# Optimization experiments

Measured on AMD Instinct MI355X. Metric: run time of the kernel, lower is better.

The kernel has to match this reference:

```python
import jax, jax.numpy as jnp
import numpy as np

LN_EPS = 1e-5

def _cell(x, h, c, Wih, Whh, bih, bhh):
    # PyTorch LSTMCell: gate order i, f, g, o
    z = x @ Wih.T + h @ Whh.T + bih + bhh
    i, f, g, o = jnp.split(z, 4, axis=-1)
    c = jax.nn.sigmoid(f) * c + jax.nn.sigmoid(i) * jnp.tanh(g)
    h = jax.nn.sigmoid(o) * jnp.tanh(c)
    return h, c

def _forward(encoder_inputs, decoder_inputs, enc_Wih, enc_Whh, enc_bih, enc_bhh,
             dec_Wih, dec_Whh, dec_bih, dec_bhh, attn_in_w, attn_in_b,
             attn_out_w, attn_out_b, ln_g, ln_b, out_w, out_b):
    B = encoder_inputs.shape[0]
    H = enc_Whh.shape[1]
    Sd = decoder_inputs.shape[1]
    h0 = jnp.zeros((B, H), encoder_inputs.dtype)
    c0 = jnp.zeros((B, H), encoder_inputs.dtype)

    def enc_step(carry, x_t):
        h, c = _cell(x_t, carry[0], carry[1], enc_Wih, enc_Whh, enc_bih, enc_bhh)
        return (h, c), h

    (h_e, c_e), hs = jax.lax.scan(enc_step, (h0, c0), jnp.swapaxes(encoder_inputs, 0, 1))
    enc_out = jnp.swapaxes(hs, 0, 1)  # [B, Se, H]

    # MultiheadAttention (1 head): precompute K, V once since keys/values are static
    Wq, Wk, Wv = jnp.split(attn_in_w, 3, axis=0)
    bq, bk, bv = jnp.split(attn_in_b, 3)
    K = enc_out @ Wk.T + bk  # [B, Se, H]
    V = enc_out @ Wv.T + bv  # [B, Se, H]
    scale = 1.0 / float(np.sqrt(H))

    def dec_step(carry, _):
        h, c, x = carry
        h, c = _cell(x, h, c, dec_Wih, dec_Whh, dec_bih, dec_bhh)
        q = h @ Wq.T + bq  # [B, H], single query per step
        attn = jax.nn.softmax(jnp.einsum('bh,bsh->bs', q, K) * scale, axis=-1)
        ctx = jnp.einsum('bs,bsh->bh', attn, V) @ attn_out_w.T + attn_out_b
        y = ctx + h  # residual with raw (pre-projection) query, as in the torch code
        mu = jnp.mean(y, axis=-1, keepdims=True)
        var = jnp.mean((y - mu) ** 2, axis=-1, keepdims=True)
        y = (y - mu) * jax.lax.rsqrt(var + LN_EPS) * ln_g + ln_b
        out = y @ out_w.T + out_b  # [B, 1]
        return (h, c, out), out

    init = (h_e, c_e, decoder_inputs[:, 0, :])
    _, outs = jax.lax.scan(dec_step, init, None, length=Sd)
    return jnp.swapaxes(outs, 0, 1)  # [B, Sd, 1]

def setup_inputs():
    key = jax.random.key(0)
    ks = jax.random.split(key, 13)
    B, Se, Sd, H, O = 64, 512, 128, 512, 1
    s = 1.0 / float(np.sqrt(H))
    def p(k, shape, sc):
        return (jax.random.uniform(k, shape, jnp.float32) * 2.0 - 1.0) * sc
    return {
        "encoder_inputs": jax.random.normal(ks[0], (B, Se, 1), jnp.float32),
        "decoder_inputs": jax.random.normal(ks[1], (B, Sd, 1), jnp.float32),
        "enc_Wih": p(ks[2], (4 * H, 1), s), "enc_Whh": p(ks[3], (4 * H, H), s),
        "enc_bih": p(ks[4], (4 * H,), s), "enc_bhh": p(ks[5], (4 * H,), s),
        "dec_Wih": p(ks[6], (4 * H, 1), s), "dec_Whh": p(ks[7], (4 * H, H), s),
        "dec_bih": p(ks[8], (4 * H,), s), "dec_bhh": p(ks[9], (4 * H,), s),
        "attn_in_w": p(ks[10], (3 * H, H), s),
        "attn_in_b": jnp.zeros((3 * H,), jnp.float32),
        "attn_out_w": p(ks[11], (H, H), s),
        "attn_out_b": jnp.zeros((H,), jnp.float32),
        "ln_g": jnp.ones((H,), jnp.float32), "ln_b": jnp.zeros((H,), jnp.float32),
        "out_w": p(ks[12], (O, H), s), "out_b": jnp.zeros((O,), jnp.float32),
    }

def reference(encoder_inputs, decoder_inputs, enc_Wih, enc_Whh, enc_bih, enc_bhh,
              dec_Wih, dec_Whh, dec_bih, dec_bhh, attn_in_w, attn_in_b,
              attn_out_w, attn_out_b, ln_g, ln_b, out_w, out_b):
    return _forward(encoder_inputs, decoder_inputs, enc_Wih, enc_Whh, enc_bih, enc_bhh,
                    dec_Wih, dec_Whh, dec_bih, dec_bhh, attn_in_w, attn_in_b,
                    attn_out_w, attn_out_b, ln_g, ln_b, out_w, out_b)
```

## Files before the change

kernel.cpp:

```cpp
#include <hip/hip_runtime.h>
#include <hip/hip_bf16.h>
#include <stdint.h>


#define HID 512
#define NBAT 64
#define SEQE 512
#define SEQD 128
#define NGRP 4
#define GBAT 16
#define GBLK 64
#define NH 8
#define SCALE 0.04419417382415922f
#define FLS 16

typedef __attribute__((ext_vector_type(8))) short bf16x8;
typedef __attribute__((ext_vector_type(4))) float f32x4;
#define MFMA_B16 __builtin_amdgcn_mfma_f32_16x16x32_bf16

static constexpr size_t OFF_G   = 0;
static constexpr size_t OFF_NM  = OFF_G  + (size_t)HID*HID*4;
static constexpr size_t OFF_M0  = OFF_NM + (size_t)HID*HID*4;
static constexpr size_t OFF_N0  = OFF_M0 + 2048;
static constexpr size_t OFF_WQB = OFF_N0 + 2048;
static constexpr size_t OFF_SC  = OFF_WQB + 2048;
static constexpr size_t OFF_HB  = OFF_SC + 256;
static constexpr size_t OFF_CB  = OFF_HB + (size_t)3*NBAT*HID*4;
static constexpr size_t OFF_EBP = OFF_CB + (size_t)NBAT*HID*4;
static constexpr size_t OFF_MD  = OFF_EBP + (size_t)NBAT*4*HID*4;
static constexpr size_t OFF_KB  = OFF_MD + (size_t)NBAT*4*4;
static constexpr size_t OFF_FLG = OFF_KB + (size_t)NBAT*SEQE*4;
static constexpr size_t OFF_XPK = OFF_FLG + (size_t)3*NGRP*GBLK*FLS*4;
static constexpr size_t OFF_BFK = ((OFF_XPK + 512 + 255) & ~(size_t)255);
static constexpr size_t OFF_BFV = OFF_BFK + (size_t)16*32*64*8*2;
static constexpr size_t OFF_EO  = OFF_BFV + (size_t)16*32*64*8*2;
static constexpr size_t OFF_VT  = OFF_EO + (size_t)NBAT*SEQE*HID*2;

__device__ __forceinline__ float bf2f(uint32_t u) {
  union { float f; uint32_t i; } x; x.i = u << 16; return x.f;
}
__device__ __forceinline__ unsigned short bfbits(float f) {
  __hip_bfloat16 h = __float2bfloat16(f);
  return *(unsigned short*)&h;
}
__device__ __forceinline__ uint32_t splitbf(float f) {
  unsigned short hi = bfbits(f);
  union { uint32_t u; float ff; } c; c.u = (uint32_t)hi << 16;
  unsigned short lo = bfbits(f - c.ff);
  return (uint32_t)hi | ((uint32_t)lo << 16);
}
__device__ __forceinline__ float sigm(float x) { return 1.f / (1.f + __expf(-x)); }

__device__ __forceinline__ void stg(float* p, float v) {
  __hip_atomic_store(p, v, __ATOMIC_RELAXED, __HIP_MEMORY_SCOPE_AGENT);
}
__device__ __forceinline__ void stgu(uint32_t* p, uint32_t v) {
  __hip_atomic_store(p, v, __ATOMIC_RELAXED, __HIP_MEMORY_SCOPE_AGENT);
}
__device__ __forceinline__ void stgi(int* p, int v) {
  __hip_atomic_store(p, v, __ATOMIC_RELAXED, __HIP_MEMORY_SCOPE_AGENT);
}
__device__ __forceinline__ void stg64(unsigned long long* p, unsigned long long v) {
  __hip_atomic_store(p, v, __ATOMIC_RELAXED, __HIP_MEMORY_SCOPE_AGENT);
}
__device__ __forceinline__ float ldg1(const float* p) {
  return __hip_atomic_load((float*)p, __ATOMIC_RELAXED, __HIP_MEMORY_SCOPE_AGENT);
}
__device__ __forceinline__ int ldgi(const int* p) {
  return __hip_atomic_load((int*)p, __ATOMIC_RELAXED, __HIP_MEMORY_SCOPE_AGENT);
}
__device__ __forceinline__ unsigned long long ldg8(const void* p) {
  return __hip_atomic_load((unsigned long long*)p, __ATOMIC_RELAXED, __HIP_MEMORY_SCOPE_AGENT);
}

#define POLL_GE(addr, thr) \
  while (ldgi(addr) < (thr)) __builtin_amdgcn_s_sleep(1);
#define CFENCE() __asm__ __volatile__("" ::: "memory")

__global__ __launch_bounds__(256) void k0_prep(
    const float* __restrict__ aiw, const float* __restrict__ aib,
    const float* __restrict__ aow, const float* __restrict__ aob,
    const float* __restrict__ outw, const float* __restrict__ lng,
    const float* __restrict__ lnb, char* __restrict__ ws) {
  float* Gm = (float*)(ws + OFF_G);
  float* Nm = (float*)(ws + OFF_NM);
  float* m0 = (float*)(ws + OFF_M0);
  float* n0 = (float*)(ws + OFF_N0);
  float* wqb = (float*)(ws + OFF_WQB);
  float* sc = (float*)(ws + OFF_SC);
  const int blk = blockIdx.x, tid = threadIdx.x;
  if (blk == 512) {
    uint32_t* hb = (uint32_t*)(ws + OFF_HB);
    int* fl = (int*)(ws + OFF_FLG);
    unsigned long long* xpk = (unsigned long long*)(ws + OFF_XPK);
    for (int i = tid; i < NBAT*HID; i += 256) hb[i] = 0u;
    for (int i = tid; i < 3*NGRP*GBLK*FLS; i += 256) {
      int set = i / (GBLK*FLS);
      fl[i] = (set >= NGRP && set < 2*NGRP) ? -1 : 0;
    }
    for (int i = tid; i < NBAT; i += 256) xpk[i] = 0ull;
    for (int l = tid; l < HID; l += 256) {
      float s = 0.f;
      for (int i = 0; i < HID; i++) s += aib[i] * aiw[(size_t)(HID + i)*HID + l];
      m0[l] = s;
    }
    for (int l = tid; l < HID; l += 256) {
      float s = 0.f;
      for (int i = 0; i < HID; i++) s += aiw[(size_t)i*HID + l] * aib[HID + i];
      wqb[l] = s;
    }
    for (int j = tid; j < HID; j += 256) {
      float s = aob[j];
      for (int i = 0; i < HID; i++) s += aow[(size_t)j*HID + i] * aib[2*HID + i];
      n0[j] = s;
    }
    __shared__ float red[256];
    float a = 0.f, b = 0.f, d = 0.f;
    for (int l = tid; l < HID; l += 256) {
      a += outw[l]*lng[l]; b += outw[l]*lnb[l]; d += aib[l]*aib[HID + l];
    }
    red[tid] = a; __syncthreads();
    for (int st = 128; st; st >>= 1) { if (tid < st) red[tid] += red[tid + st]; __syncthreads(); }
    if (tid == 0) sc[0] = red[0];
    __syncthreads();
    red[tid] = b; __syncthreads();
    for (int st = 128; st; st >>= 1) { if (tid < st) red[tid] += red[tid + st]; __syncthreads(); }
    if (tid == 0) sc[1] = red[0];
    __syncthreads();
    red[tid] = d; __syncthreads();
    for (int st = 128; st; st >>= 1) { if (tid < st) red[tid] += red[tid + st]; __syncthreads(); }
    if (tid == 0) sc[2] = red[0];
    return;
  }
  const bool isG = blk < 256;
  const int tb = isG ? blk : blk - 256;
  const int r0 = (tb >> 4) * 32, c0 = (tb & 15) * 32;
  __shared__ float sa[32][33], sb[32][33];
  float acc[4] = {0.f, 0.f, 0.f, 0.f};
  const int tr = tid >> 3, tc = (tid & 7) * 4;
  for (int i0 = 0; i0 < HID; i0 += 32) {
    __syncthreads();
    if (isG) {
      for (int j = 0; j < 4; j++) sa[tr][tc + j] = aiw[(size_t)(HID + i0 + tr)*HID + r0 + tc + j];
      for (int j = 0; j < 4; j++) sb[tr][tc + j] = aiw[(size_t)(i0 + tr)*HID + c0 + tc + j];
    } else {
      for (int j = 0; j < 4; j++) sa[tr][tc + j] = aow[(size_t)(r0 + tr)*HID + i0 + tc + j];
      for (int j = 0; j < 4; j++) sb[tr][tc + j] = aiw[(size_t)(2*HID + i0 + tr)*HID + c0 + tc + j];
    }
    __syncthreads();
    if (isG) {
      for (int i = 0; i < 32; i++) {
        float a = sa[i][tr];
        for (int j = 0; j < 4; j++) acc[j] += a * sb[i][tc + j];
      }
    } else {
      for (int i = 0; i < 32; i++) {
        float a = sa[tr][i];
        for (int j = 0; j < 4; j++) acc[j] += a * sb[i][tc + j];
      }
    }
  }
  float* dst = isG ? Gm : Nm;
  for (int j = 0; j < 4; j++) dst[(size_t)(r0 + tr)*HID + c0 + tc + j] = acc[j];
}

__global__ __launch_bounds__(256) void k0b_frag(char* __restrict__ ws) {
  const float* Gm = (const float*)(ws + OFF_G);
  const float* Nm = (const float*)(ws + OFF_NM);
  unsigned short* Bfk = (unsigned short*)(ws + OFF_BFK);
  unsigned short* Bfv = (unsigned short*)(ws + OFF_BFV);
  const int idx0 = blockIdx.x * 256 + threadIdx.x;
  for (int idx = idx0; idx < 16*32*64; idx += 64*256) {
    int ks = idx >> 11, lt = (idx >> 6) & 31, l = idx & 63;
    int lcol = lt*16 + (l & 15), krow = ks*32 + ((l >> 4) << 3);
    unsigned short hk[8] __attribute__((aligned(16)));
    unsigned short hv[8] __attribute__((aligned(16)));
    for (int j = 0; j < 8; j++) {
      hk[j] = bfbits(Gm[(size_t)(krow + j)*HID + lcol]);
      hv[j] = bfbits(Nm[(size_t)lcol*HID + krow + j]);
    }
    *(uint4*)(Bfk + (size_t)idx*8) = *(uint4*)hk;
    *(uint4*)(Bfv + (size_t)idx*8) = *(uint4*)hv;
  }
}

#define STAGE_FULL8(srcPTR)                                                           \
  {                                                                                   \
    const unsigned long long* _s = (const unsigned long long*)(srcPTR);               \
    unsigned long long _tm[8];                                                        \
    _Pragma("unroll") for (int r = 0; r < 8; r++) _tm[r] = ldg8(_s + tid + r*512);    \
    _Pragma("unroll") for (int r = 0; r < 8; r++) {                                   \
      int i = tid + r*512;                                                            \
      int bb_ = i >> 8, kk = (i & 255) * 2;                                           \
      unsigned long long u = _tm[r];                                                  \
      *(uint32_t*)&s_hh[bb_][kk] = (uint32_t)(u & 0xffffu) | (((uint32_t)(u >> 32) & 0xffffu) << 16); \
      *(uint32_t*)&s_hl[bb_][kk] = ((uint32_t)(u >> 16) & 0xffffu) | ((uint32_t)(u >> 48) << 16);     \
    }                                                                                 \
  }

#define STAGE_SLICE8(srcPTR)                                                          \
  {                                                                                   \
    const unsigned long long* _s = (const unsigned long long*)(srcPTR);               \
    const int _half = l >> 5, _co = wv*32 + (l & 31);                                 \
    unsigned long long _tm[8];                                                        \
    _Pragma("unroll") for (int r = 0; r < 8; r++)                                     \
      _tm[r] = ldg8(_s + (size_t)(_half*8 + r)*(HID/2) + _co);                        \
    const int kk = _co*2;                                                             \
    _Pragma("unroll") for (int r = 0; r < 8; r++) {                                   \
      unsigned long long u = _tm[r];                                                  \
      int bb_ = _half*8 + r;                                                          \
      *(uint32_t*)&s_hh[bb_][kk] = (uint32_t)(u & 0xffffu) | (((uint32_t)(u >> 32) & 0xffffu) << 16); \
      *(uint32_t*)&s_hl[bb_][kk] = ((uint32_t)(u >> 16) & 0xffffu) | ((uint32_t)(u >> 48) << 16);     \
    }                                                                                 \
  }

#define WFRAG_INIT_512()                                                              \
  for (int slot = tid; slot < 2*16*64; slot += 512) {                                 \
    int T = slot >> 10, ks = (slot >> 6) & 15, l_ = slot & 63;                        \
    int rloc = T*16 + (l_ & 15);                                                      \
    int grow = (rloc >> 3)*HID + hs + (rloc & 7);                                     \
    int ko = ks*32 + ((l_ >> 4) << 3);                                                \
    const float* wp = &whh[(size_t)grow*HID + ko];                                    \
    unsigned short hi[8] __attribute__((aligned(16)));                                \
    unsigned short lo[8] __attribute__((aligned(16)));                                \
    for (int j = 0; j < 8; j++) {                                                     \
      uint32_t u = splitbf(wp[j]);                                                    \
      hi[j] = (unsigned short)u; lo[j] = (unsigned short)(u >> 16);                   \
    }                                                                                 \
    *(uint4*)&s_wf[T][ks][l_][0] = *(uint4*)hi;                                       \
    *(uint4*)&s_wl[T][ks][l_][0] = *(uint4*)lo;                                       \
  }

#define CELL_MFMA8()                                                                  \
  {                                                                                   \
    f32x4 acc0 = {0.f,0.f,0.f,0.f}, acc1 = {0.f,0.f,0.f,0.f};                         \
    _Pragma("unroll") for (int kq = 0; kq < 2; kq++) {                                \
      const int ks = wv*2 + kq;                                                       \
      const int ko = ks*32 + (oc << 3);                                               \
      bf16x8 ahi = *(const bf16x8*)&s_hh[lm][ko];                                     \
      bf16x8 alo = *(const bf16x8*)&s_hl[lm][ko];                                     \
      bf16x8 b0h = *(const bf16x8*)&s_wf[0][ks][l][0];                                \
      bf16x8 b0l = *(const bf16x8*)&s_wl[0][ks][l][0];                                \
      bf16x8 b1h = *(const bf16x8*)&s_wf[1][ks][l][0];                                \
      bf16x8 b1l = *(const bf16x8*)&s_wl[1][ks][l][0];                                \
      acc0 = MFMA_B16(ahi, b0h, acc0, 0, 0, 0);                                       \
      acc0 = MFMA_B16(alo, b0h, acc0, 0, 0, 0);                                       \
      acc0 = MFMA_B16(ahi, b0l, acc0, 0, 0, 0);                                       \
      acc1 = MFMA_B16(ahi, b1h, acc1, 0, 0, 0);                                       \
      acc1 = MFMA_B16(alo, b1h, acc1, 0, 0, 0);                                       \
      acc1 = MFMA_B16(ahi, b1l, acc1, 0, 0, 0);                                       \
    }                                                                                 \
    _Pragma("unroll") for (int q = 0; q < 4; q++) {                                   \
      int idx = (oc*4 + q)*16 + lm;                                                   \
      s_pacc[wv][0][idx] = acc0[q];                                                   \
      s_pacc[wv][1][idx] = acc1[q];                                                   \
    }                                                                                 \
  }                                                                                   \
  __syncthreads();

#define CELL_MFMA8R()                                                                 \
  {                                                                                   \
    f32x4 acc0 = {0.f,0.f,0.f,0.f}, acc1 = {0.f,0.f,0.f,0.f};                         \
    _Pragma("unroll") for (int kq = 0; kq < 2; kq++) {                                \
      const int ks = wv*2 + kq;                                                       \
      const int ko = ks*32 + (oc << 3);                                               \
      bf16x8 ahi = *(const bf16x8*)&s_hh[lm][ko];                                     \
      bf16x8 alo = *(const bf16x8*)&s_hl[lm][ko];                                     \
      acc0 = MFMA_B16(ahi, wh0[kq], acc0, 0, 0, 0);                                   \
      acc0 = MFMA_B16(alo, wh0[kq], acc0, 0, 0, 0);                                   \
      acc0 = MFMA_B16(ahi, wl0[kq], acc0, 0, 0, 0);                                   \
      acc1 = MFMA_B16(ahi, wh1[kq], acc1, 0, 0, 0);                                   \
      acc1 = MFMA_B16(alo, wh1[kq], acc1, 0, 0, 0);                                   \
      acc1 = MFMA_B16(ahi, wl1[kq], acc1, 0, 0, 0);                                   \
    }                                                                                 \
    _Pragma("unroll") for (int q = 0; q < 4; q++) {                                   \
      int idx = (oc*4 + q)*16 + lm;                                                   \
      s_pacc[wv][0][idx] = acc0[q];                                                   \
      s_pacc[wv][1][idx] = acc1[q];                                                   \
    }                                                                                 \
  }                                                                                   \
  __syncthreads();

#define GATES_SUM()                                                                   \
      float zi = 0.f, zf = 0.f, zg = 0.f, zo = 0.f;                                   \
      _Pragma("unroll") for (int w = 0; w < 8; w++) {                                 \
        zi += s_pacc[w][0][b*16+j];                                                   \
        zf += s_pacc[w][0][b*16+8+j];                                                 \
        zg += s_pacc[w][1][b*16+j];                                                   \
        zo += s_pacc[w][1][b*16+8+j];                                                 \
      }                                                                               \
      float x = s_x[b];                                                               \
      zi += x*s_wih[j]    + s_bias[j];                                                \
      zf += x*s_wih[8+j]  + s_bias[8+j];                                              \
      zg += x*s_wih[16+j] + s_bias[16+j];                                             \
      zo += x*s_wih[24+j] + s_bias[24+j];

__global__ __launch_bounds__(512) void k1_enc(
    const float* __restrict__ xin, const float* __restrict__ wih,
    const float* __restrict__ whh, const float* __restrict__ bih,
    const float* __restrict__ bhh, char* __restrict__ ws) {
  const int bk = blockIdx.x, tid = threadIdx.x;
  const int g = bk >> 6, jb = bk & 63;
  const int hs = jb * NH, b0 = g * GBAT;
  uint32_t* hbuf = (uint32_t*)(ws + OFF_HB);
  float* cbuf = (float*)(ws + OFF_CB);
  unsigned short* eo = (unsigned short*)(ws + OFF_EO);
  int* fl = (int*)(ws + OFF_FLG) + g * GBLK * FLS;

  __shared__ __align__(16) unsigned short s_wf[2][16][64][8];
  __shared__ __align__(16) unsigned short s_wl[2][16][64][8];
  __shared__ __align__(16) unsigned short s_hh[GBAT][520];
  __shared__ __align__(16) unsigned short s_hl[GBAT][520];
  __shared__ float s_pacc[8][2][256];
  __shared__ float s_c[GBAT][NH];
  __shared__ float s_x[GBAT];
  __shared__ float s_wih[32], s_bias[32];

  WFRAG_INIT_512()
  if (tid < 32) {
    int grow = (tid >> 3)*HID + hs + (tid & 7);
    s_wih[tid] = wih[grow];
    s_bias[tid] = bih[grow] + bhh[grow];
  }
  for (int i = tid; i < GBAT*NH; i += 512) s_c[i >> 3][i & 7] = 0.f;

  const int l = tid & 63, wv = tid >> 6;
  const int lm = l & 15, oc = l >> 4;

  for (int t = 0; t < SEQE; t++) {
    if (tid < GBAT) s_x[tid] = xin[(size_t)(b0 + tid)*SEQE + t];
    if (l < 8) { POLL_GE(&fl[(wv*8 + l)*FLS], t) }
    CFENCE();
    STAGE_SLICE8(hbuf + (size_t)(t % 3)*NBAT*HID + (size_t)b0*HID)
    CELL_MFMA8()
    if (tid < GBLK) { POLL_GE(&fl[tid*FLS], t - 1) }
    __syncthreads();
    if (tid < 128) {
      int b = tid >> 3, j = tid & 7;
      GATES_SUM()
      float c = s_c[b][j];
      c = sigm(zf)*c + sigm(zi)*tanhf(zg);
      float hv = sigm(zo)*tanhf(c);
      s_c[b][j] = c;
      uint32_t pk = splitbf(hv);
      stgu(&hbuf[(size_t)((t+1)%3)*NBAT*HID + (size_t)(b0+b)*HID + hs + j], pk);
      eo[((size_t)(b0+b)*SEQE + t)*HID + hs + j] = (unsigned short)(pk & 0xffffu);
    }
    __syncthreads();
    if (tid == 0) stgi(&fl[jb*FLS], t + 1);
  }
  if (tid < GBAT*NH)
    cbuf[(size_t)(b0 + (tid >> 3))*HID + hs + (tid & 7)] = s_c[tid >> 3][tid & 7];
}

__global__ __launch_bounds__(256) void k0c_kv(char* __restrict__ ws) {
  const float* wqb = (const float*)(ws + OFF_WQB);
  const float* m0 = (const float*)(ws + OFF_M0);
  const float* scv = (const float*)(ws + OFF_SC);
  const unsigned short* Bfk = (const unsigned short*)(ws + OFF_BFK);
  const unsigned short* Bfv = (const unsigned short*)(ws + OFF_BFV);
  unsigned short* eoK = (unsigned short*)(ws + OFF_EO);
  unsigned short* Vt = (unsigned short*)(ws + OFF_VT);
  float* kbv = (float*)(ws + OFF_KB);
  const int b = blockIdx.x >> 4, s0 = (blockIdx.x & 15) * 32;
  const int tid = threadIdx.x;
  __shared__ __align__(16) unsigned short s_e[32][520];
  __shared__ float s_kb[32][8];
  {
    const uint4* src = (const uint4*)(eoK + ((size_t)b*SEQE + s0)*HID);
    #pragma unroll
    for (int r = 0; r < 8; r++) {
      int i = tid + r*256;
      uint4 v = src[i];
      int rr = i >> 6, cc = (i & 63)*8;
      *(uint4*)&s_e[rr][cc] = v;
    }
  }
  __syncthreads();
  const int l = tid & 63, wv = tid >> 6, lm = l & 15, oc = l >> 4;
  for (int nt = 0; nt < 8; nt++) {
    const int lt = wv*8 + nt;
    f32x4 accK0 = {0,0,0,0}, accK1 = {0,0,0,0}, accV0 = {0,0,0,0}, accV1 = {0,0,0,0};
    #pragma unroll
    for (int ks = 0; ks < 16; ks++) {
      bf16x8 yk = *(const bf16x8*)(Bfk + (((size_t)ks*32 + lt)*64 + l)*8);
      bf16x8 yv = *(const bf16x8*)(Bfv + (((size_t)ks*32 + lt)*64 + l)*8);
      bf16x8 xe0 = *(const bf16x8*)&s_e[lm][ks*32 + oc*8];
      bf16x8 xe1 = *(const bf16x8*)&s_e[16 + lm][ks*32 + oc*8];
      accK0 = MFMA_B16(xe0, yk, accK0, 0,0,0);
      accK1 = MFMA_B16(xe1, yk, accK1, 0,0,0);
      accV0 = MFMA_B16(xe0, yv, accV0, 0,0,0);
      accV1 = MFMA_B16(xe1, yv, accV1, 0,0,0);
    }
    const float wq = wqb[lt*16 + lm];
    #pragma unroll
    for (int st = 0; st < 2; st++) {
      const f32x4& aK = st ? accK1 : accK0;
      const f32x4& aV = st ? accV1 : accV0;
      #pragma unroll
      for (int q = 0; q < 4; q++)
        eoK[((size_t)b*SEQE + s0 + st*16 + oc*4 + q)*HID + lt*16 + lm] = bfbits(aK[q] + wq);
      unsigned short pv[4] __attribute__((aligned(8)));
      #pragma unroll
      for (int q = 0; q < 4; q++) pv[q] = bfbits(aV[q]);
      *(unsigned long long*)(Vt + ((size_t)b*HID + lt*16 + lm)*SEQE + s0 + st*16 + oc*4)
          = *(unsigned long long*)pv;
    }
  }
  {
    int s = tid >> 3, kc = tid & 7;
    float acc = 0.f;
    for (int i = 0; i < 64; i++) {
      int k = kc*64 + i;
      acc += bf2f((uint32_t)s_e[s][k]) * m0[k];
    }
    s_kb[s][kc] = acc;
  }
  __syncthreads();
  if (tid < 32) {
    float a = 0.f;
    for (int kc = 0; kc < 8; kc++) a += s_kb[tid][kc];
    kbv[(size_t)b*SEQE + s0 + tid] = a + scv[2];
  }
}

__global__ __launch_bounds__(512) void k2_dec(
    const float* __restrict__ xin, const float* __restrict__ wih,
    const float* __restrict__ whh, const float* __restrict__ bih,
    const float* __restrict__ bhh, const float* __restrict__ lng,
    const float* __restrict__ lnb, const float* __restrict__ outw,
    const float* __restrict__ outb, char* __restrict__ ws,
    float* __restrict__ dout) {
  const int bk = blockIdx.x, tid = threadIdx.x;
  const int g = bk >> 6, jb = bk & 63;
  const int hs = jb * NH, b0 = g * GBAT;
  uint32_t* hbuf = (uint32_t*)(ws + OFF_HB);
  float* cbuf = (float*)(ws + OFF_CB);
  float* ebp  = (float*)(ws + OFF_EBP);
  float* md   = (float*)(ws + OFF_MD);
  const float* n0v = (const float*)(ws + OFF_N0);
  const float* scv = (const float*)(ws + OFF_SC);
  const float* kbv = (const float*)(ws + OFF_KB);
  const unsigned short* Kt = (const unsigned short*)(ws + OFF_EO);
  const unsigned short* Vt = (const unsigned short*)(ws + OFF_VT);
  unsigned long long* xpk = (unsigned long long*)(ws + OFF_XPK);
  int* fl2 = (int*)(ws + OFF_FLG) + (NGRP + g) * GBLK * FLS;
  int* pfl = (int*)(ws + OFF_FLG) + (2*NGRP + g) * GBLK * FLS;

  __shared__ __align__(16) unsigned short s_hh[GBAT][520];
  __shared__ __align__(16) unsigned short s_hl[GBAT][520];
  __shared__ __align__(16) unsigned short s_kt[64][520];
  __shared__ float s_pacc[8][2][256];
  __shared__ float s_c[GBAT][NH];
  __shared__ float s_x[GBAT];
  __shared__ float s_wih[32], s_bias[32];
  __shared__ float s_scores[128];
  __shared__ __align__(16) uint32_t s_pbf[64];
  __shared__ float s_red[32];
  __shared__ float s_ln[HID], s_n0f[HID];

  const int l = tid & 63, wv = tid >> 6;
  const int lm = l & 15, oc = l >> 4;
  const int bb = jb >> 2, scq = jb & 3, batch = b0 + bb;

  bf16x8 wh0[2], wl0[2], wh1[2], wl1[2];
  #pragma unroll
  for (int kq = 0; kq < 2; kq++) {
    const int ks = wv*2 + kq;
    #pragma unroll
    for (int T = 0; T < 2; T++) {
      int rloc = T*16 + lm;
      int grow = (rloc >> 3)*HID + hs + (rloc & 7);
      const float* wp = &whh[(size_t)grow*HID + ks*32 + oc*8];
      unsigned short hi8[8] __attribute__((aligned(16)));
      unsigned short lo8[8] __attribute__((aligned(16)));
      #pragma unroll
      for (int j = 0; j < 8; j++) {
        uint32_t u = splitbf(wp[j]);
        hi8[j] = (unsigned short)u; lo8[j] = (unsigned short)(u >> 16);
      }
      if (T == 0) { wh0[kq] = *(bf16x8*)hi8; wl0[kq] = *(bf16x8*)lo8; }
      else        { wh1[kq] = *(bf16x8*)hi8; wl1[kq] = *(bf16x8*)lo8; }
    }
  }
  bf16x8 vreg[4][4];
  {
    const unsigned short* vp = Vt + (size_t)batch*HID*SEQE + (size_t)scq*128;
    #pragma unroll
    for (int n = 0; n < 4; n++)
      #pragma unroll
      for (int ks = 0; ks < 4; ks++)
        vreg[n][ks] = *(const bf16x8*)(vp + (size_t)((wv*4 + n)*16 + lm)*SEQE + ks*32 + oc*8);
  }
  for (int i = tid; i < 4096; i += 512) {
    int row = i >> 6, cc = (i & 63) * 8;
    *(uint4*)&s_kt[row][cc] =
        *(const uint4*)(Kt + ((size_t)batch*SEQE + scq*128 + row)*HID + cc);
  }

  if (tid < 32) {
    int grow = (tid >> 3)*HID + hs + (tid & 7);
    s_wih[tid] = wih[grow];
    s_bias[tid] = bih[grow] + bhh[grow];
  }
  for (int i = tid; i < HID; i += 512) {
    s_ln[i] = outw[i] * lng[i];
    s_n0f[i] = n0v[i];
  }
  for (int i = tid; i < GBAT*NH; i += 512)
    s_c[i >> 3][i & 7] = cbuf[(size_t)(b0 + (i >> 3))*HID + hs + (i & 7)];
  const float Swg = scv[0], Swb = scv[1], ob0 = outb[0];

  STAGE_FULL8(hbuf + (size_t)2*NBAT*HID + (size_t)b0*HID)
  if (tid < GBAT) s_x[tid] = xin[(size_t)(b0 + tid)*SEQD];
  __syncthreads();
  if (tid == 0) stgi(&fl2[jb*FLS], 0);

  for (int t = 0; t < SEQD; t++) {
    CELL_MFMA8R()
    if (tid < GBLK) { POLL_GE(&fl2[tid*FLS], t - 1) }
    __syncthreads();
    if (tid < 128) {
      int b = tid >> 3, j = tid & 7;
      GATES_SUM()
      float c = s_c[b][j];
      c = sigm(zf)*c + sigm(zi)*tanhf(zg);
      float hv = sigm(zo)*tanhf(c);
      s_c[b][j] = c;
      stgu(&hbuf[(size_t)((t+1)%3)*NBAT*HID + (size_t)(b0+b)*HID + hs + j], splitbf(hv));
    }
    __syncthreads();
    if (tid == 0) stgi(&fl2[jb*FLS], t + 1);
    if (l < 8) { POLL_GE(&fl2[(wv*8 + l)*FLS], t + 1) }
    CFENCE();
    STAGE_SLICE8(hbuf + (size_t)((t+1)%3)*NBAT*HID + (size_t)b0*HID)
    __syncthreads();
    {
      f32x4 acc = {0.f,0.f,0.f,0.f};
      if (wv < 4) {
        #pragma unroll
        for (int ks = 0; ks < 16; ks++) {
          bf16x8 xh = *(const bf16x8*)&s_hh[bb][ks*32 + oc*8];
          bf16x8 yk = *(const bf16x8*)&s_kt[wv*16 + lm][ks*32 + oc*8];
          acc = MFMA_B16(xh, yk, acc, 0, 0, 0);
        }
      } else {
        const unsigned short* kp =
            Kt + ((size_t)batch*SEQE + scq*128 + 64 + (wv - 4)*16)*HID;
        #pragma unroll
        for (int ks = 0; ks < 16; ks++) {
          bf16x8 xh = *(const bf16x8*)&s_hh[bb][ks*32 + oc*8];
          bf16x8 yk = *(const bf16x8*)(kp + (size_t)lm*HID + ks*32 + oc*8);
          acc = MFMA_B16(xh, yk, acc, 0, 0, 0);
        }
      }
      if (oc == 0) s_scores[wv*16 + lm] = acc[0];
    }
    __syncthreads();
    float den_part = 0.f;
    if (tid < 128) {
      float sv = (s_scores[tid] + kbv[(size_t)batch*SEQE + scq*128 + tid]) * SCALE;
      den_part = __expf(sv);
      s_scores[tid] = den_part;
    }
    __syncthreads();
    if (tid < 64)
      s_pbf[tid] = (uint32_t)bfbits(s_scores[2*tid]) | ((uint32_t)bfbits(s_scores[2*tid+1]) << 16);
    if (tid < 128) {
      for (int off = 32; off; off >>= 1) den_part += __shfl_down(den_part, off);
      if ((tid & 63) == 0) s_red[tid >> 6] = den_part;
    }
    __syncthreads();
    if (tid == 0) stg(&md[batch*4 + scq], s_red[0] + s_red[1]);
    {
      #pragma unroll
      for (int n = 0; n < 4; n++) {
        const int lv0 = (wv*4 + n)*16;
        f32x4 acc = {0.f,0.f,0.f,0.f};
        #pragma unroll
        for (int ks = 0; ks < 4; ks++) {
          bf16x8 xp = *(const bf16x8*)((const unsigned short*)s_pbf + ks*32 + oc*8);
          acc = MFMA_B16(xp, vreg[n][ks], acc, 0, 0, 0);
        }
        if (oc == 0) stg(&ebp[((size_t)batch*4 + scq)*HID + lv0 + lm], acc[0]);
      }
    }
    __syncthreads();
    if (tid == 0) stgi(&pfl[jb*FLS], t + 1);
    if (jb < GBAT) {
      #pragma unroll
      for (int q = 0; q < 4; q++) { POLL_GE(&pfl[(4*jb + q)*FLS], t + 1) }
      CFENCE();
      const int mb = b0 + jb;
      if (tid < 4) s_red[tid] = ldg1(&md[mb*4 + tid]);
      __syncthreads();
      const float inv = 1.f / (s_red[0] + s_red[1] + s_red[2] + s_red[3]);
      if (tid < 256) {
        float sy = 0.f, sy2 = 0.f, sg = 0.f;
        #pragma unroll
        for (int u = 0; u < 2; u++) {
          const int lv = tid*2 + u;
          float p0 = ldg1(&ebp[((size_t)mb*4 + 0)*HID + lv]);
          float p1 = ldg1(&ebp[((size_t)mb*4 + 1)*HID + lv]);
          float p2 = ldg1(&ebp[((size_t)mb*4 + 2)*HID + lv]);
          float p3 = ldg1(&ebp[((size_t)mb*4 + 3)*HID + lv]);
          float hval = bf2f((uint32_t)s_hh[jb][lv]) + bf2f((uint32_t)s_hl[jb][lv]);
          float y = (p0 + p1 + p2 + p3)*inv + s_n0f[lv] + hval;
          sy += y; sy2 += y*y; sg += s_ln[lv]*y;
        }
        for (int off = 32; off; off >>= 1) {
          sy += __shfl_down(sy, off); sy2 += __shfl_down(sy2, off); sg += __shfl_down(sg, off);
        }
        if (l == 0) { s_red[8+wv] = sy; s_red[12+wv] = sy2; s_red[16+wv] = sg; }
      }
      __syncthreads();
      if (tid == 0) {
        float Sy  = s_red[8]  + s_red[9]  + s_red[10] + s_red[11];
        float Sy2 = s_red[12] + s_red[13] + s_red[14] + s_red[15];
        float Sg  = s_red[16] + s_red[17] + s_red[18] + s_red[19];
        float mu = Sy * (1.f/HID);
        float var = Sy2 * (1.f/HID) - mu*mu;
        float rs = rsqrtf(var + 1e-5f);
        float o = rs*(Sg - mu*Swg) + Swb + ob0;
        dout[(size_t)mb*SEQD + t] = o;
        union { float f; uint32_t u; } cv; cv.f = o;
        stg64(&xpk[mb], ((unsigned long long)cv.u << 32) | (uint32_t)(t + 1));
      }
    }
    if (tid < GBAT) {
      unsigned long long v;
      do { v = ldg8(&xpk[b0 + tid]); __builtin_amdgcn_s_sleep(1); }
      while ((uint32_t)v < (uint32_t)(t + 1));
      union { uint32_t u; float f; } cv; cv.u = (uint32_t)(v >> 32);
      s_x[tid] = cv.f;
    }
    CFENCE();
  }
}

extern "C" void kernel_launch(void* const* d_in, const int* in_sizes, int n_in,
                              void* d_out, int out_size, void* d_ws, size_t ws_size,
                              hipStream_t stream) {
  const float* enc_in = (const float*)d_in[0];
  const float* dec_in = (const float*)d_in[1];
  const float* ewih = (const float*)d_in[2];
  const float* ewhh = (const float*)d_in[3];
  const float* ebih = (const float*)d_in[4];
  const float* ebhh = (const float*)d_in[5];
  const float* dwih = (const float*)d_in[6];
  const float* dwhh = (const float*)d_in[7];
  const float* dbih = (const float*)d_in[8];
  const float* dbhh = (const float*)d_in[9];
  const float* aiw  = (const float*)d_in[10];
  const float* aib  = (const float*)d_in[11];
  const float* aow  = (const float*)d_in[12];
  const float* aob  = (const float*)d_in[13];
  const float* lng  = (const float*)d_in[14];
  const float* lnb  = (const float*)d_in[15];
  const float* outw = (const float*)d_in[16];
  const float* outb = (const float*)d_in[17];
  char* ws = (char*)d_ws;
  k0_prep<<<513, 256, 0, stream>>>(aiw, aib, aow, aob, outw, lng, lnb, ws);
  k0b_frag<<<64, 256, 0, stream>>>(ws);
  k1_enc<<<256, 512, 0, stream>>>(enc_in, ewih, ewhh, ebih, ebhh, ws);
  k0c_kv<<<1024, 256, 0, stream>>>(ws);
  k2_dec<<<256, 512, 0, stream>>>(dec_in, dwih, dwhh, dbih, dbhh,
                                  lng, lnb, outw, outb, ws, (float*)d_out);
}
```

Baseline: 3.024 ms.

## Replace encoder step flags with tagged hidden-state packets and double-buffered partials

The encoder recurrence no longer polls per-block progress flags. Each hidden-state packet now carries a 2-bit step tag in its low bits, and consumers spin on the data itself until the tag matches. Two adjacent hidden units are packed per 64-bit word, the partial-sum scratch is double-buffered by step parity so one barrier can go, and the decoder's initial staging is adapted to the new packed format. This aims to cut the flag round-trip and barrier latency on every sequential step. In exchange it steals low mantissa bits of the low-order bf16 half, which risks precision and relies on 64-bit store atomicity for tag visibility.

```diff
diff --git a/kernel.cpp b/kernel.cpp
--- a/kernel.cpp
+++ b/kernel.cpp
@@ -93,7 +93,7 @@
     uint32_t* hb = (uint32_t*)(ws + OFF_HB);
     int* fl = (int*)(ws + OFF_FLG);
     unsigned long long* xpk = (unsigned long long*)(ws + OFF_XPK);
-    for (int i = tid; i < NBAT*HID; i += 256) hb[i] = 0u;
+    for (int i = tid; i < 3*NBAT*HID; i += 256) hb[i] = 0u;
     for (int i = tid; i < 3*NGRP*GBLK*FLS; i += 256) {
       int set = i / (GBLK*FLS);
       fl[i] = (set >= NGRP && set < 2*NGRP) ? -1 : 0;
@@ -184,17 +184,38 @@
   }
 }
 
-#define STAGE_FULL8(srcPTR)                                                           \
+#define STAGE_TAGGED(SLOT, TAGV)                                                      \
   {                                                                                   \
-    const unsigned long long* _s = (const unsigned long long*)(srcPTR);               \
-    unsigned long long _tm[8];                                                        \
-    _Pragma("unroll") for (int r = 0; r < 8; r++) _tm[r] = ldg8(_s + tid + r*512);    \
+    const unsigned long long* _s = hb64 + ((size_t)(SLOT)*NBAT + b0)*(HID/2);         \
+    const int _b = l >> 2, _pb = wv*32 + (l & 3)*8;                                   \
+    unsigned long long _v[8];                                                         \
+    _Pragma("unroll") for (int r = 0; r < 8; r++)                                     \
+      _v[r] = ldg8(_s + (size_t)_b*(HID/2) + _pb + r);                                \
     _Pragma("unroll") for (int r = 0; r < 8; r++) {                                   \
-      int i = tid + r*512;                                                            \
-      int bb_ = i >> 8, kk = (i & 255) * 2;                                           \
-      unsigned long long u = _tm[r];                                                  \
-      *(uint32_t*)&s_hh[bb_][kk] = (uint32_t)(u & 0xffffu) | (((uint32_t)(u >> 32) & 0xffffu) << 16); \
-      *(uint32_t*)&s_hl[bb_][kk] = ((uint32_t)(u >> 16) & 0xffffu) | ((uint32_t)(u >> 48) << 16);     \
+      while ((int)(_v[r] & 3) != (TAGV)) {                                            \
+        __builtin_amdgcn_s_sleep(1);                                                  \
+        _v[r] = ldg8(_s + (size_t)_b*(HID/2) + _pb + r);                              \
+      }                                                                               \
+    }                                                                                 \
+    _Pragma("unroll") for (int r = 0; r < 8; r++) {                                   \
+      unsigned long long u = _v[r];                                                   \
+      uint32_t hi2 = (uint32_t)((u >> 48) & 0xffffu) | ((uint32_t)((u >> 32) & 0xffffu) << 16); \
+      uint32_t lo2 = ((uint32_t)((u >> 17) & 0x7fffu) << 1) | ((uint32_t)((u >> 2) & 0x7fffu) << 17); \
+      *(uint32_t*)&s_hh[_b][(_pb + r)*2] = hi2;                                       \
+      *(uint32_t*)&s_hl[_b][(_pb + r)*2] = lo2;                                       \
+    }                                                                                 \
+  }
+
+#define STAGE_FULL_PAIR(SLOT)                                                         \
+  {                                                                                   \
+    const unsigned long long* _s = hb64 + ((size_t)(SLOT)*NBAT + b0)*(HID/2);         \
+    const int _b = tid >> 5, _pb = (tid & 31)*8;                                      \
+    _Pragma("unroll") for (int r = 0; r < 8; r++) {                                   \
+      unsigned long long u = ldg8(_s + (size_t)_b*(HID/2) + _pb + r);                 \
+      uint32_t hi2 = (uint32_t)((u >> 48) & 0xffffu) | ((uint32_t)((u >> 32) & 0xffffu) << 16); \
+      uint32_t lo2 = ((uint32_t)((u >> 17) & 0x7fffu) << 1) | ((uint32_t)((u >> 2) & 0x7fffu) << 17); \
+      *(uint32_t*)&s_hh[_b][(_pb + r)*2] = hi2;                                       \
+      *(uint32_t*)&s_hl[_b][(_pb + r)*2] = lo2;                                       \
     }                                                                                 \
   }
 
@@ -231,7 +252,7 @@
     *(uint4*)&s_wl[T][ks][l_][0] = *(uint4*)lo;                                       \
   }
 
-#define CELL_MFMA8()                                                                  \
+#define CELL_MFMA8(PAR)                                                               \
   {                                                                                   \
     f32x4 acc0 = {0.f,0.f,0.f,0.f}, acc1 = {0.f,0.f,0.f,0.f};                         \
     _Pragma("unroll") for (int kq = 0; kq < 2; kq++) {                                \
@@ -252,8 +273,8 @@
     }                                                                                 \
     _Pragma("unroll") for (int q = 0; q < 4; q++) {                                   \
       int idx = (oc*4 + q)*16 + lm;                                                   \
-      s_pacc[wv][0][idx] = acc0[q];                                                   \
-      s_pacc[wv][1][idx] = acc1[q];                                                   \
+      s_pacc[PAR][wv][0][idx] = acc0[q];                                              \
+      s_pacc[PAR][wv][1][idx] = acc1[q];                                              \
     }                                                                                 \
   }                                                                                   \
   __syncthreads();
@@ -281,6 +302,38 @@
   }                                                                                   \
   __syncthreads();
 
+#define GATES2(PACC, SLOT, TAGV, EO_STORE)                                            \
+  if (tid < 64) {                                                                     \
+    const int b = tid >> 2, jp = tid & 3;                                             \
+    const int j0 = jp*2, j1 = jp*2 + 1;                                               \
+    float x = s_x[b];                                                                 \
+    float zi0=0.f,zf0=0.f,zg0=0.f,zo0=0.f, zi1=0.f,zf1=0.f,zg1=0.f,zo1=0.f;           \
+    _Pragma("unroll") for (int w = 0; w < 8; w++) {                                   \
+      zi0 += PACC[w][0][b*16+j0];   zf0 += PACC[w][0][b*16+8+j0];                     \
+      zg0 += PACC[w][1][b*16+j0];   zo0 += PACC[w][1][b*16+8+j0];                     \
+      zi1 += PACC[w][0][b*16+j1];   zf1 += PACC[w][0][b*16+8+j1];                     \
+      zg1 += PACC[w][1][b*16+j1];   zo1 += PACC[w][1][b*16+8+j1];                     \
+    }                                                                                 \
+    zi0 += x*s_wih[j0]    + s_bias[j0];    zi1 += x*s_wih[j1]    + s_bias[j1];        \
+    zf0 += x*s_wih[8+j0]  + s_bias[8+j0];  zf1 += x*s_wih[8+j1]  + s_bias[8+j1];      \
+    zg0 += x*s_wih[16+j0] + s_bias[16+j0]; zg1 += x*s_wih[16+j1] + s_bias[16+j1];     \
+    zo0 += x*s_wih[24+j0] + s_bias[24+j0]; zo1 += x*s_wih[24+j1] + s_bias[24+j1];     \
+    float c0 = s_c[b][j0];                                                            \
+    c0 = sigm(zf0)*c0 + sigm(zi0)*tanhf(zg0);                                         \
+    float h0v = sigm(zo0)*tanhf(c0); s_c[b][j0] = c0;                                 \
+    float c1 = s_c[b][j1];                                                            \
+    c1 = sigm(zf1)*c1 + sigm(zi1)*tanhf(zg1);                                         \
+    float h1v = sigm(zo1)*tanhf(c1); s_c[b][j1] = c1;                                 \
+    uint32_t sa = splitbf(h0v), sb2 = splitbf(h1v);                                   \
+    unsigned long long pk = ((unsigned long long)(sa & 0xffffu) << 48)                \
+                          | ((unsigned long long)(sb2 & 0xffffu) << 32)               \
+                          | ((unsigned long long)((sa >> 17) & 0x7fffu) << 17)        \
+                          | ((unsigned long long)((sb2 >> 17) & 0x7fffu) << 2)        \
+                          | (unsigned long long)(TAGV);                               \
+    stg64(&hb64[((size_t)(SLOT)*NBAT + b0 + b)*(HID/2) + jb*4 + jp], pk);             \
+    EO_STORE                                                                          \
+  }
+
 #define GATES_SUM()                                                                   \
       float zi = 0.f, zf = 0.f, zg = 0.f, zo = 0.f;                                   \
       _Pragma("unroll") for (int w = 0; w < 8; w++) {                                 \
@@ -302,16 +355,15 @@
   const int bk = blockIdx.x, tid = threadIdx.x;
   const int g = bk >> 6, jb = bk & 63;
   const int hs = jb * NH, b0 = g * GBAT;
-  uint32_t* hbuf = (uint32_t*)(ws + OFF_HB);
+  unsigned long long* hb64 = (unsigned long long*)(ws + OFF_HB);
   float* cbuf = (float*)(ws + OFF_CB);
   unsigned short* eo = (unsigned short*)(ws + OFF_EO);
-  int* fl = (int*)(ws + OFF_FLG) + g * GBLK * FLS;
 
   __shared__ __align__(16) unsigned short s_wf[2][16][64][8];
   __shared__ __align__(16) unsigned short s_wl[2][16][64][8];
   __shared__ __align__(16) unsigned short s_hh[GBAT][520];
   __shared__ __align__(16) unsigned short s_hl[GBAT][520];
-  __shared__ float s_pacc[8][2][256];
+  __shared__ float s_pacc[2][8][2][256];
   __shared__ float s_c[GBAT][NH];
   __shared__ float s_x[GBAT];
   __shared__ float s_wih[32], s_bias[32];
@@ -323,32 +375,20 @@
     s_bias[tid] = bih[grow] + bhh[grow];
   }
   for (int i = tid; i < GBAT*NH; i += 512) s_c[i >> 3][i & 7] = 0.f;
+  __syncthreads();
 
   const int l = tid & 63, wv = tid >> 6;
   const int lm = l & 15, oc = l >> 4;
 
   for (int t = 0; t < SEQE; t++) {
     if (tid < GBAT) s_x[tid] = xin[(size_t)(b0 + tid)*SEQE + t];
-    if (l < 8) { POLL_GE(&fl[(wv*8 + l)*FLS], t) }
-    CFENCE();
-    STAGE_SLICE8(hbuf + (size_t)(t % 3)*NBAT*HID + (size_t)b0*HID)
-    CELL_MFMA8()
-    if (tid < GBLK) { POLL_GE(&fl[tid*FLS], t - 1) }
-    __syncthreads();
-    if (tid < 128) {
-      int b = tid >> 3, j = tid & 7;
-      GATES_SUM()
-      float c = s_c[b][j];
-      c = sigm(zf)*c + sigm(zi)*tanhf(zg);
-      float hv = sigm(zo)*tanhf(c);
-      s_c[b][j] = c;
-      uint32_t pk = splitbf(hv);
-      stgu(&hbuf[(size_t)((t+1)%3)*NBAT*HID + (size_t)(b0+b)*HID + hs + j], pk);
-      eo[((size_t)(b0+b)*SEQE + t)*HID + hs + j] = (unsigned short)(pk & 0xffffu);
-    }
-    __syncthreads();
-    if (tid == 0) stgi(&fl[jb*FLS], t + 1);
-  }
+    STAGE_TAGGED(t % 3, t & 3)
+    CELL_MFMA8(t & 1)
+    GATES2(s_pacc[t & 1], (t+1) % 3, (t+1) & 3,
+      { *(uint32_t*)&eo[((size_t)(b0+b)*SEQE + t)*HID + hs + j0] =
+            (sa & 0xffffu) | ((sb2 & 0xffffu) << 16); })
+  }
+  __syncthreads();
   if (tid < GBAT*NH)
     cbuf[(size_t)(b0 + (tid >> 3))*HID + hs + (tid & 7)] = s_c[tid >> 3][tid & 7];
 }
@@ -435,6 +475,7 @@
   const int g = bk >> 6, jb = bk & 63;
   const int hs = jb * NH, b0 = g * GBAT;
   uint32_t* hbuf = (uint32_t*)(ws + OFF_HB);
+  unsigned long long* hb64 = (unsigned long long*)(ws + OFF_HB);
   float* cbuf = (float*)(ws + OFF_CB);
   float* ebp  = (float*)(ws + OFF_EBP);
   float* md   = (float*)(ws + OFF_MD);
@@ -497,7 +538,6 @@
     *(uint4*)&s_kt[row][cc] =
         *(const uint4*)(Kt + ((size_t)batch*SEQE + scq*128 + row)*HID + cc);
   }
-
   if (tid < 32) {
     int grow = (tid >> 3)*HID + hs + (tid & 7);
     s_wih[tid] = wih[grow];
@@ -511,7 +551,7 @@
     s_c[i >> 3][i & 7] = cbuf[(size_t)(b0 + (i >> 3))*HID + hs + (i & 7)];
   const float Swg = scv[0], Swb = scv[1], ob0 = outb[0];
 
-  STAGE_FULL8(hbuf + (size_t)2*NBAT*HID + (size_t)b0*HID)
+  STAGE_FULL_PAIR(2)
   if (tid < GBAT) s_x[tid] = xin[(size_t)(b0 + tid)*SEQD];
   __syncthreads();
   if (tid == 0) stgi(&fl2[jb*FLS], 0);
```

New measurement: 6.476 ms. 2.14x slower.
